# Kernel optimization log

Hardware: AMD Instinct MI355X
Metric: run time of the kernel (lower is better)

The kernel has to match this reference:

```python
import jax, jax.numpy as jnp
import numpy as np

B, T, P = 64, 512, 8
V, O, E, H, C_SIZE = 50000, 50000, 512, 2048, 5
A1, A2, A3, A4, A5 = 1.0, 0.5, 0.5, 0.5, 0.5


def setup_inputs() -> dict:
    key = jax.random.key(0)
    ks = jax.random.split(key, 8)
    s = 0.02
    return dict(
        encoder_output=jax.random.normal(ks[0], (B, H), jnp.float32),
        predict_sequence=jax.random.randint(ks[1], (B, P), 0, 500),
        source=jax.random.randint(ks[2], (B, T), 0, 500),
        source_lens=jax.random.randint(ks[3], (B,), T // 2, T + 1),
        E_table=jax.random.normal(ks[4], (V, E), jnp.float32) * s,
        W1=jax.random.normal(ks[5], (C_SIZE * E, H), jnp.float32) * s,
        b1=jnp.zeros((H,), jnp.float32),
        W2=jax.random.normal(ks[6], (H, O), jnp.float32) * s,
        b2=jnp.zeros((O,), jnp.float32),
        W3=jax.random.normal(ks[7], (H, O), jnp.float32) * s,
        b3=jnp.zeros((O,), jnp.float32),
    )


def _features(predict_sequence, source, source_lens):
    # Vectorized replacement of the per-sample Python n-gram/reorder loop.
    b, t = source.shape
    mask = jnp.arange(t)[None, :] < source_lens[:, None]          # valid positions [B,T]
    w1 = predict_sequence[:, -1]                                  # last predicted token
    w2a = predict_sequence[:, -2]                                 # second-to-last
    # bigram: exists p with source[p]==w1 and source[p+1]==source[pos]
    first2 = source[:, :-1] == w1[:, None]                        # [B,T-1]
    eq2 = source[:, :, None] == source[:, None, 1:]               # [B,T,T-1]
    big = jnp.any(eq2 & first2[:, None, :], axis=-1)              # [B,T]
    # trigram: exists p with source[p]==w2a, source[p+1]==w1, source[p+2]==source[pos]
    first3 = (source[:, :-2] == w2a[:, None]) & (source[:, 1:-1] == w1[:, None])
    eq3 = source[:, :, None] == source[:, None, 2:]               # [B,T,T-2]
    tri = jnp.any(eq3 & first3[:, None, :], axis=-1)
    # reordering: first index of source[pos] < first index of w1 (when w1 present)
    eqw = source == w1[:, None]
    in_list = jnp.any(eqw, axis=-1)
    kpos = jnp.argmax(eqw, axis=-1)                               # first occurrence of w1
    jpos = jnp.argmax(source[:, :, None] == source[:, None, :], axis=-1)  # first occ. of each id
    reo = in_list[:, None] & (jpos < kpos[:, None])
    rows = jnp.broadcast_to(jnp.arange(b)[:, None], (b, t))
    def scat(flags):
        return jnp.zeros((b, O), jnp.float32).at[rows, source].max((flags & mask).astype(jnp.float32))
    return scat(mask), scat(big), scat(tri), scat(reo)


def reference(encoder_output, predict_sequence, source, source_lens,
              E_table, W1, b1, W2, b2, W3, b3):
    bsz = encoder_output.shape[0]
    ctx = E_table[predict_sequence[:, -C_SIZE:]].reshape(bsz, -1)  # [B, C*E]
    h = jnp.tanh(ctx @ W1 + b1)                                    # [B, H]
    out = (h @ W2 + b2) + (encoder_output @ W3 + b3)               # Vh + Wenc
    uni, big, tri, reo = _features(predict_sequence, source, source_lens)
    comb = out * A1 + uni * A2 + big * A3 + tri * A4 + reo * A5
    return jax.nn.softmax(comb, axis=1)
```

## Files before the change

kernel.cpp:

```cpp
#include <hip/hip_runtime.h>
#include <math.h>

#define BSZ   64
#define TLEN  512
#define ODIM  50000
#define HDIM  2048
#define K1DIM 2560
#define K2DIM 4096
#define KSPLIT 5

typedef __bf16 bf16x8 __attribute__((ext_vector_type(8)));
typedef float f32x4 __attribute__((ext_vector_type(4)));

__device__ __forceinline__ unsigned short f2b(float f) {
    unsigned int u = __float_as_uint(f);
    u += 0x7FFFu + ((u >> 16) & 1u);
    return (unsigned short)(u >> 16);
}

__device__ __forceinline__ bf16x8 ld_bf16x8(const unsigned short* p) {
    union { uint4 u; bf16x8 v; } x;
    x.u = *reinterpret_cast<const uint4*>(p);
    return x.v;
}

__global__ __launch_bounds__(256) void prep_kernel(
    const float* __restrict__ enc, const int* __restrict__ ps,
    const float* __restrict__ Et, unsigned short* __restrict__ ctx,
    unsigned short* __restrict__ A2)
{
    int i = blockIdx.x * 256 + threadIdx.x;
    const int NE = BSZ * HDIM;
    if (i < NE) {
        int m = i >> 11, j = i & (HDIM - 1);
        A2[m * K2DIM + HDIM + j] = f2b(enc[i]);
    } else {
        int t = i - NE;
        int m = t / K1DIM, j = t - m * K1DIM;
        int c = j >> 9, e = j & 511;
        int tok = ps[m * 8 + 3 + c];
        ctx[m * K1DIM + j] = f2b(Et[(size_t)tok * 512 + e]);
    }
}

__global__ __launch_bounds__(256) void gemm1_kernel(
    const unsigned short* __restrict__ Actx, const float* __restrict__ W1,
    float* __restrict__ part)
{
    int n0 = blockIdx.x * 64;
    int ks = blockIdx.y;
    int wave = threadIdx.x >> 6;
    int lane = threadIdx.x & 63;
    int q = lane >> 4, l16 = lane & 15;
    int ncol = n0 + wave * 16 + l16;

    f32x4 acc[4] = {};
    for (int kk = 0; kk < 16; ++kk) {
        int kq = ks * 512 + kk * 32 + q * 8;
        const unsigned short* ap = Actx + l16 * K1DIM + kq;
        bf16x8 a0 = ld_bf16x8(ap);
        bf16x8 a1 = ld_bf16x8(ap + 16 * K1DIM);
        bf16x8 a2 = ld_bf16x8(ap + 32 * K1DIM);
        bf16x8 a3 = ld_bf16x8(ap + 48 * K1DIM);
        const float* wp = W1 + (size_t)kq * HDIM + ncol;
        union { unsigned short s[8]; bf16x8 v; } bb;
#pragma unroll
        for (int j = 0; j < 8; ++j) { bb.s[j] = f2b(*wp); wp += HDIM; }
        acc[0] = __builtin_amdgcn_mfma_f32_16x16x32_bf16(a0, bb.v, acc[0], 0, 0, 0);
        acc[1] = __builtin_amdgcn_mfma_f32_16x16x32_bf16(a1, bb.v, acc[1], 0, 0, 0);
        acc[2] = __builtin_amdgcn_mfma_f32_16x16x32_bf16(a2, bb.v, acc[2], 0, 0, 0);
        acc[3] = __builtin_amdgcn_mfma_f32_16x16x32_bf16(a3, bb.v, acc[3], 0, 0, 0);
    }
    float* pp = part + (size_t)ks * (BSZ * HDIM);
#pragma unroll
    for (int mt = 0; mt < 4; ++mt)
#pragma unroll
        for (int r = 0; r < 4; ++r)
            pp[(mt * 16 + q * 4 + r) * HDIM + ncol] = acc[mt][r];
}

__global__ __launch_bounds__(256) void htanh_kernel(
    const float* __restrict__ part, const float* __restrict__ b1,
    unsigned short* __restrict__ A2)
{
    int i = blockIdx.x * 256 + threadIdx.x;
    int m = i >> 11, n = i & (HDIM - 1);
    float s = b1[n];
#pragma unroll
    for (int ks = 0; ks < KSPLIT; ++ks) s += part[(size_t)ks * (BSZ * HDIM) + m * HDIM + n];
    A2[m * K2DIM + n] = f2b(tanhf(s));
}

__global__ __launch_bounds__(256) void gemm2_kernel(
    const unsigned short* __restrict__ A, const float* __restrict__ W2,
    const float* __restrict__ W3, const float* __restrict__ b2,
    const float* __restrict__ b3, float* __restrict__ out)
{
    int bid = blockIdx.x;
    int xcd = bid & 7;
    int slot = bid >> 3;
    int tile = xcd * 98 + slot;
    int n0 = tile * 64;
    if (n0 >= ODIM) return;
    int wave = threadIdx.x >> 6;
    int lane = threadIdx.x & 63;
    int q = lane >> 4, l16 = lane & 15;
    int ncol = n0 + wave * 16 + l16;
    int nc = ncol < ODIM ? ncol : (ODIM - 1);

    f32x4 acc[4] = {};
    for (int k0 = 0; k0 < K2DIM; k0 += 32) {
        int kq = k0 + q * 8;
        const unsigned short* ap = A + l16 * K2DIM + kq;
        bf16x8 a0 = ld_bf16x8(ap);
        bf16x8 a1 = ld_bf16x8(ap + 16 * K2DIM);
        bf16x8 a2 = ld_bf16x8(ap + 32 * K2DIM);
        bf16x8 a3 = ld_bf16x8(ap + 48 * K2DIM);
        const float* W = (k0 < HDIM) ? W2 : W3;
        int kr = (k0 < HDIM) ? kq : (kq - HDIM);
        const float* wp = W + (size_t)kr * ODIM + nc;
        union { unsigned short s[8]; bf16x8 v; } bb;
#pragma unroll
        for (int j = 0; j < 8; ++j) { bb.s[j] = f2b(*wp); wp += ODIM; }
        acc[0] = __builtin_amdgcn_mfma_f32_16x16x32_bf16(a0, bb.v, acc[0], 0, 0, 0);
        acc[1] = __builtin_amdgcn_mfma_f32_16x16x32_bf16(a1, bb.v, acc[1], 0, 0, 0);
        acc[2] = __builtin_amdgcn_mfma_f32_16x16x32_bf16(a2, bb.v, acc[2], 0, 0, 0);
        acc[3] = __builtin_amdgcn_mfma_f32_16x16x32_bf16(a3, bb.v, acc[3], 0, 0, 0);
    }
    if (ncol < ODIM) {
        float bias = b2[ncol] + b3[ncol];
#pragma unroll
        for (int mt = 0; mt < 4; ++mt)
#pragma unroll
            for (int r = 0; r < 4; ++r)
                out[(size_t)(mt * 16 + q * 4 + r) * ODIM + ncol] = acc[mt][r] + bias;
    }
}

__global__ __launch_bounds__(256) void feats_kernel(
    const int* __restrict__ src_g, const int* __restrict__ lens,
    const int* __restrict__ ps, float* __restrict__ out)
{
    __shared__ int src[TLEN];
    int b = blockIdx.x;
    int tid = threadIdx.x;
    for (int t = tid; t < TLEN; t += 256) src[t] = src_g[b * TLEN + t];
    __syncthreads();
    int len = lens[b];
    int w1 = ps[b * 8 + 7];
    int w2a = ps[b * 8 + 6];

    for (int t = tid; t < TLEN; t += 256) {
        int v = src[t];
        bool first = true, big = false, tri = false;
        int kp = TLEN;
        for (int j = 0; j < TLEN; ++j) {
            int sj = src[j];
            int sj1 = (j < TLEN - 1) ? src[j + 1] : -1;
            int sj2 = (j < TLEN - 2) ? src[j + 2] : -1;
            if (j < t && sj == v) first = false;
            if (sj == w1 && sj1 == v) big = true;
            if (sj == w2a && sj1 == w1 && sj2 == v) tri = true;
            if (sj == w1 && j < kp) kp = j;
        }
        if (t < len && first) {
            bool in_list = kp < TLEN;
            bool reo = in_list && (t < kp);
            float add = 0.5f * (1.0f + (big ? 1.0f : 0.0f) + (tri ? 1.0f : 0.0f) + (reo ? 1.0f : 0.0f));
            out[(size_t)b * ODIM + v] += add;
        }
    }
}

__global__ __launch_bounds__(256) void rowstats_kernel(
    const float* __restrict__ out, float* __restrict__ stats)
{
    int b = blockIdx.x, tid = threadIdx.x;
    const float* row = out + (size_t)b * ODIM;
    float m = -INFINITY, s = 0.0f;
    for (int i = tid; i < ODIM; i += 256) {
        float x = row[i];
        if (x > m) { s = s * __expf(m - x) + 1.0f; m = x; }
        else s += __expf(x - m);
    }
    __shared__ float ms[256], ss[256];
    ms[tid] = m; ss[tid] = s;
    __syncthreads();
    for (int off = 128; off > 0; off >>= 1) {
        if (tid < off) {
            float m1 = ms[tid], s1 = ss[tid];
            float m2 = ms[tid + off], s2 = ss[tid + off];
            float M = fmaxf(m1, m2);
            ss[tid] = s1 * __expf(m1 - M) + s2 * __expf(m2 - M);
            ms[tid] = M;
        }
        __syncthreads();
    }
    if (tid == 0) { stats[b] = ms[0]; stats[64 + b] = ss[0]; }
}

__global__ __launch_bounds__(256) void norm_kernel(
    float* __restrict__ out, const float* __restrict__ stats)
{
    int i = blockIdx.x * 256 + threadIdx.x;
    int row = i / 12500;
    int off = i - row * 12500;
    float m = stats[row];
    float inv = 1.0f / stats[64 + row];
    float4* p = reinterpret_cast<float4*>(out + (size_t)row * ODIM) + off;
    float4 x = *p;
    x.x = __expf(x.x - m) * inv;
    x.y = __expf(x.y - m) * inv;
    x.z = __expf(x.z - m) * inv;
    x.w = __expf(x.w - m) * inv;
    *p = x;
}

extern "C" void kernel_launch(void* const* d_in, const int* in_sizes, int n_in,
                              void* d_out, int out_size, void* d_ws, size_t ws_size,
                              hipStream_t stream) {
    const float* enc  = (const float*)d_in[0];
    const int*   ps   = (const int*)d_in[1];
    const int*   src  = (const int*)d_in[2];
    const int*   lens = (const int*)d_in[3];
    const float* Et   = (const float*)d_in[4];
    const float* W1   = (const float*)d_in[5];
    const float* b1   = (const float*)d_in[6];
    const float* W2   = (const float*)d_in[7];
    const float* b2   = (const float*)d_in[8];
    const float* W3   = (const float*)d_in[9];
    const float* b3   = (const float*)d_in[10];
    float* out = (float*)d_out;

    char* ws = (char*)d_ws;
    unsigned short* ctx = (unsigned short*)(ws);
    unsigned short* A2  = (unsigned short*)(ws + 524288);
    float* part         = (float*)(ws + 1048576);
    float* stats        = (float*)(ws + 3801088);

    prep_kernel<<<1152, 256, 0, stream>>>(enc, ps, Et, ctx, A2);
    gemm1_kernel<<<dim3(32, KSPLIT), 256, 0, stream>>>(ctx, W1, part);
    htanh_kernel<<<512, 256, 0, stream>>>(part, b1, A2);
    gemm2_kernel<<<784, 256, 0, stream>>>(A2, W2, W3, b2, b3, out);
    feats_kernel<<<64, 256, 0, stream>>>(src, lens, ps, out);
    rowstats_kernel<<<64, 256, 0, stream>>>(out, stats);
    norm_kernel<<<3125, 256, 0, stream>>>(out, stats);
}
```

Baseline: 1.248 ms.

## Stage W2/W3 tiles through double-buffered LDS with coalesced float4 loads

The gemm2 kernel now loads 64-row K tiles of W2/W3 with coalesced float4 global reads, converts them to bf16, and writes them into a double-buffered LDS tile. Each wave then gathers B fragments from LDS. This replaces the strided per-element global loads, one scalar per ODIM stride. The next tile is prefetched into registers while the current one is computed, so global latency overlaps the MFMA work. In exchange it adds a __syncthreads per tile and some LDS bank traffic from the 2-byte column reads. Edge columns are clamped so the float4 loads stay in bounds.

Measured after the change: 1.170 ms. -6.2%, faster.

```diff
diff --git a/kernel.cpp b/kernel.cpp
--- a/kernel.cpp
+++ b/kernel.cpp
@@ -91,42 +91,85 @@
     A2[m * K2DIM + n] = f2b(tanhf(s));
 }
 
+#define KT 64
+#define SKB 136
+#define BUFB (KT * SKB)
+
 __global__ __launch_bounds__(256) void gemm2_kernel(
     const unsigned short* __restrict__ A, const float* __restrict__ W2,
     const float* __restrict__ W3, const float* __restrict__ b2,
     const float* __restrict__ b3, float* __restrict__ out)
 {
+    __shared__ char lds[2 * BUFB];
     int bid = blockIdx.x;
-    int xcd = bid & 7;
-    int slot = bid >> 3;
-    int tile = xcd * 98 + slot;
+    int tile = (bid & 7) * 98 + (bid >> 3);
+    if (tile >= 782) return;
     int n0 = tile * 64;
-    if (n0 >= ODIM) return;
-    int wave = threadIdx.x >> 6;
-    int lane = threadIdx.x & 63;
+
+    int tid = threadIdx.x;
+    int wave = tid >> 6;
+    int lane = tid & 63;
     int q = lane >> 4, l16 = lane & 15;
     int ncol = n0 + wave * 16 + l16;
-    int nc = ncol < ODIM ? ncol : (ODIM - 1);
+    int nloc = wave * 16 + l16;
+
+    int rr = tid >> 4;
+    int cg = tid & 15;
+    int gcol = n0 + cg * 4;
+    if (gcol > ODIM - 4) gcol = ODIM - 4;
+
+    float4 stage[4];
+#pragma unroll
+    for (int r = 0; r < 4; ++r) {
+        int krow = r * 16 + rr;
+        stage[r] = *reinterpret_cast<const float4*>(W2 + (size_t)krow * ODIM + gcol);
+    }
 
     f32x4 acc[4] = {};
-    for (int k0 = 0; k0 < K2DIM; k0 += 32) {
-        int kq = k0 + q * 8;
-        const unsigned short* ap = A + l16 * K2DIM + kq;
-        bf16x8 a0 = ld_bf16x8(ap);
-        bf16x8 a1 = ld_bf16x8(ap + 16 * K2DIM);
-        bf16x8 a2 = ld_bf16x8(ap + 32 * K2DIM);
-        bf16x8 a3 = ld_bf16x8(ap + 48 * K2DIM);
-        const float* W = (k0 < HDIM) ? W2 : W3;
-        int kr = (k0 < HDIM) ? kq : (kq - HDIM);
-        const float* wp = W + (size_t)kr * ODIM + nc;
-        union { unsigned short s[8]; bf16x8 v; } bb;
-#pragma unroll
-        for (int j = 0; j < 8; ++j) { bb.s[j] = f2b(*wp); wp += ODIM; }
-        acc[0] = __builtin_amdgcn_mfma_f32_16x16x32_bf16(a0, bb.v, acc[0], 0, 0, 0);
-        acc[1] = __builtin_amdgcn_mfma_f32_16x16x32_bf16(a1, bb.v, acc[1], 0, 0, 0);
-        acc[2] = __builtin_amdgcn_mfma_f32_16x16x32_bf16(a2, bb.v, acc[2], 0, 0, 0);
-        acc[3] = __builtin_amdgcn_mfma_f32_16x16x32_bf16(a3, bb.v, acc[3], 0, 0, 0);
-    }
+    const unsigned short* abase = A + l16 * K2DIM;
+
+    for (int kt = 0; kt < 64; ++kt) {
+        char* buf = lds + (kt & 1) * BUFB;
+#pragma unroll
+        for (int r = 0; r < 4; ++r) {
+            union { unsigned short s[4]; unsigned long long u; } pk;
+            pk.s[0] = f2b(stage[r].x);
+            pk.s[1] = f2b(stage[r].y);
+            pk.s[2] = f2b(stage[r].z);
+            pk.s[3] = f2b(stage[r].w);
+            *reinterpret_cast<unsigned long long*>(buf + (r * 16 + rr) * SKB + cg * 8) = pk.u;
+        }
+        __syncthreads();
+        if (kt + 1 < 64) {
+            int kg0 = (kt + 1) * KT;
+#pragma unroll
+            for (int r = 0; r < 4; ++r) {
+                int krow = kg0 + r * 16 + rr;
+                const float* src = (krow < HDIM) ? (W2 + (size_t)krow * ODIM)
+                                                 : (W3 + (size_t)(krow - HDIM) * ODIM);
+                stage[r] = *reinterpret_cast<const float4*>(src + gcol);
+            }
+        }
+#pragma unroll
+        for (int h = 0; h < 2; ++h) {
+            int kq = kt * KT + h * 32 + q * 8;
+            const unsigned short* ap = abase + kq;
+            bf16x8 a0 = ld_bf16x8(ap);
+            bf16x8 a1 = ld_bf16x8(ap + 16 * K2DIM);
+            bf16x8 a2 = ld_bf16x8(ap + 32 * K2DIM);
+            bf16x8 a3 = ld_bf16x8(ap + 48 * K2DIM);
+            union { unsigned short s[8]; bf16x8 v; } bb;
+            const char* bp = buf + (h * 32 + q * 8) * SKB + nloc * 2;
+#pragma unroll
+            for (int j = 0; j < 8; ++j)
+                bb.s[j] = *reinterpret_cast<const unsigned short*>(bp + j * SKB);
+            acc[0] = __builtin_amdgcn_mfma_f32_16x16x32_bf16(a0, bb.v, acc[0], 0, 0, 0);
+            acc[1] = __builtin_amdgcn_mfma_f32_16x16x32_bf16(a1, bb.v, acc[1], 0, 0, 0);
+            acc[2] = __builtin_amdgcn_mfma_f32_16x16x32_bf16(a2, bb.v, acc[2], 0, 0, 0);
+            acc[3] = __builtin_amdgcn_mfma_f32_16x16x32_bf16(a3, bb.v, acc[3], 0, 0, 0);
+        }
+    }
+
     if (ncol < ODIM) {
         float bias = b2[ncol] + b3[ncol];
 #pragma unroll
```
